# Optimization experiments

Measured on AMD Instinct MI355X. Metric: run time of the kernel, lower is better.

Reference implementation:

```python
import jax, jax.numpy as jnp
import numpy as np

NR, NS = 4, 3      # num_rotations, num_scales
RP, SP = 2, 2      # rotation_size, scale_size
K = 5              # kernel_size
PAD = 2
STRIDE = 1
NF = 9             # num basis functions (effective_size**2)


def setup_inputs() -> dict:
    key = jax.random.key(0)
    k1, k2, k3 = jax.random.split(key, 3)
    x = jax.random.normal(k1, (8, 16, NR * NS, 128, 128), dtype=jnp.float32)
    weight = jax.random.normal(k2, (16, 16, RP * SP, NF), dtype=jnp.float32) * 0.05
    basis = jax.random.normal(k3, (NF, NR * NS, K, K), dtype=jnp.float32)
    return {"x": x, "weight": weight, "basis": basis}


def reference(x, weight, basis):
    B, C, S, H, W = x.shape
    out_c, in_c, _, nf = weight.shape
    nrs = NR * NS
    # kernel synthesis: weight @ basis -> [nrs, out, in, RP*SP, K, K]
    kernel = jnp.einsum('oirf,fgxy->goirxy', weight, basis)
    kernel = kernel.reshape(nrs * out_c, in_c, RP, SP, K, K)
    # reshape input to [B, C, NR, NS, H, W]
    xg = x.reshape(B, C, NR, NS, H, W)
    # zero-pad scale axis at the end by SP-1
    xg = jnp.pad(xg, ((0, 0), (0, 0), (0, 0), (0, SP - 1), (0, 0), (0, 0)))
    # circular-pad rotation axis at the end by RP-1 (wrap from beginning)
    xg = jnp.concatenate([xg, xg[:, :, :RP - 1]], axis=2)
    out = None
    for i in range(RP):
        for j in range(SP):
            xs = xg[:, :, i:i + NR, j:j + NS]                     # [B,C,NR,NS,H,W]
            xs = xs.transpose(0, 2, 3, 1, 4, 5).reshape(B, nrs * C, H, W)
            o = jax.lax.conv_general_dilated(
                xs, kernel[:, :, i, j],
                window_strides=(STRIDE, STRIDE),
                padding=[(PAD, PAD), (PAD, PAD)],
                feature_group_count=nrs,
                dimension_numbers=('NCHW', 'OIHW', 'NCHW'))
            out = o if out is None else out + o
    B_, C_, H_, W_ = out.shape
    out = out.reshape(B_, nrs, out_c, H_, W_).transpose(0, 2, 1, 3, 4)
    return out
```

## Files before the change

kernel.cpp:

```cpp
#include <hip/hip_runtime.h>


#define NRS 12
#define CIN 16
#define COUT 16
#define HW 128
#define IMG (HW*HW)
#define ICSTRIDE (NRS*IMG)
#define HALO_H 36
#define HALO_W 20
#define NPIX (HALO_H*HALO_W)
#define HALFBYTES (NPIX*8*2)
#define ROWB (HALO_W*16)

typedef __bf16 bf16x8 __attribute__((ext_vector_type(8)));
typedef float  f32x4  __attribute__((ext_vector_type(4)));

__device__ __forceinline__ unsigned short f2bf(float f) {
    unsigned u = __builtin_bit_cast(unsigned, f);
    u += 0x7fffu + ((u >> 16) & 1u);
    return (unsigned short)(u >> 16);
}

__global__ void build_kc(const float* __restrict__ wgt, const float* __restrict__ basis,
                         unsigned short* __restrict__ kc) {
    int idx = blockIdx.x * 256 + threadIdx.x;
    const int total = 12 * 4 * 13 * 16 * 32;
    if (idx >= total) return;
    int k  = idx & 31;
    int possel = k >> 4, ic = k & 15;
    int o  = (idx >> 5) & 15;
    int t2 = idx >> 9;
    int pp = t2 % 13;
    int gr = t2 / 13;
    int rbase = gr & 3, g = gr >> 2;
    int pos = 2 * pp + possel;
    float s = 0.f;
    if (pos < 25) {
        int xk = pos / 5, yk = pos - 5 * xk;
        #pragma unroll
        for (int f = 0; f < 9; ++f)
            s = fmaf(wgt[((o * CIN + ic) * 4 + rbase) * 9 + f],
                     basis[((f * NRS + g) * 5 + xk) * 5 + yk], s);
    }
    kc[idx] = f2bf(s);
}

__global__ __launch_bounds__(256, 2)
void conv_mfma(const float* __restrict__ x, const unsigned short* __restrict__ kc,
               float* __restrict__ out) {
    const int b   = blockIdx.z;
    const int r0  = blockIdx.y;
    const int th0 = (blockIdx.x >> 3) * 32;
    const int tw0 = (blockIdx.x & 7) * 16;

    const int t    = threadIdx.x;
    const int lane = t & 63;
    const int wave = t >> 6;
    const int n    = lane & 15;
    const int q    = lane >> 4;
    const int possel = q >> 1;
    const int half_  = q & 1;

    __shared__ uint4 xs4[(2 * HALFBYTES) / 16];
    char* xsc = (char*)xs4;

    int boff[13];
    #pragma unroll
    for (int pp = 0; pp < 13; ++pp) {
        int pos = 2 * pp + possel; if (pos > 24) pos = 24;
        int dx = pos / 5, dy = pos - 5 * dx;
        boff[pp] = half_ * HALFBYTES + dx * ROWB + (n + dy) * 16;
    }
    const int aoff = n * 32 + q * 8;

    f32x4 acc[3][8];
    #pragma unroll
    for (int s0 = 0; s0 < 3; ++s0)
        #pragma unroll
        for (int pg = 0; pg < 8; ++pg) acc[s0][pg] = (f32x4){0.f, 0.f, 0.f, 0.f};

    #pragma unroll 1
    for (int i = 0; i < 2; ++i) {
        int rr = r0 + i; if (rr >= 4) rr -= 4;
        #pragma unroll
        for (int ss = 0; ss < 3; ++ss) {
            const int sin_ = rr * 3 + ss;
            const float* xb = x + ((size_t)b * CIN * NRS + sin_) * IMG;

            __syncthreads();
            for (int p = t; p < NPIX; p += 256) {
                int rl = p / HALO_W, cl = p - rl * HALO_W;
                int hh = th0 + rl - 2, ww = tw0 + cl - 2;
                bool ok = ((unsigned)hh < 128u) && ((unsigned)ww < 128u);
                const float* px = xb + hh * HW + ww;
                unsigned short v[16];
                #pragma unroll
                for (int ic = 0; ic < 16; ++ic) {
                    float f = 0.f;
                    if (ok) f = px[(size_t)ic * ICSTRIDE];
                    v[ic] = f2bf(f);
                }
                uint4 lo, hi;
                lo.x = v[0] | (v[1] << 16);  lo.y = v[2] | (v[3] << 16);
                lo.z = v[4] | (v[5] << 16);  lo.w = v[6] | (v[7] << 16);
                hi.x = v[8] | (v[9] << 16);  hi.y = v[10] | (v[11] << 16);
                hi.z = v[12] | (v[13] << 16); hi.w = v[14] | (v[15] << 16);
                *(uint4*)(xsc + p * 16)             = lo;
                *(uint4*)(xsc + HALFBYTES + p * 16) = hi;
            }
            __syncthreads();

            const unsigned short* kc0 = kc + (size_t)((r0 * 3 + ss) * 4 + 2 * i) * (13 * 512);
            const unsigned short* kc1 = kc + (size_t)((r0 * 3 + ss - 1) * 4 + 2 * i + 1) * (13 * 512);
            const char* wb = xsc + wave * 8 * ROWB;
            #pragma unroll
            for (int pp = 0; pp < 13; ++pp) {
                bf16x8 af0 = *(const bf16x8*)(kc0 + pp * 512 + aoff);
                bf16x8 af1;
                if (ss > 0) af1 = *(const bf16x8*)(kc1 + pp * 512 + aoff);
                const char* wp = wb + boff[pp];
                #pragma unroll
                for (int pg = 0; pg < 8; ++pg) {
                    bf16x8 bfv = *(const bf16x8*)(wp + pg * ROWB);
                    acc[ss][pg] = __builtin_amdgcn_mfma_f32_16x16x32_bf16(af0, bfv, acc[ss][pg], 0, 0, 0);
                    if (ss > 0)
                        acc[ss - 1][pg] = __builtin_amdgcn_mfma_f32_16x16x32_bf16(af1, bfv, acc[ss - 1][pg], 0, 0, 0);
                }
            }
        }
    }

    #pragma unroll
    for (int s0 = 0; s0 < 3; ++s0) {
        const size_t obase = ((size_t)b * COUT * NRS + (r0 * 3 + s0)) * IMG;
        #pragma unroll
        for (int pg = 0; pg < 8; ++pg) {
            int row = th0 + wave * 8 + pg;
            int col = tw0 + n;
            size_t pix = (size_t)row * HW + col;
            #pragma unroll
            for (int r = 0; r < 4; ++r) {
                int o = q * 4 + r;
                out[obase + (size_t)o * NRS * IMG + pix] = acc[s0][pg][r];
            }
        }
    }
}

extern "C" void kernel_launch(void* const* d_in, const int* in_sizes, int n_in,
                              void* d_out, int out_size, void* d_ws, size_t ws_size,
                              hipStream_t stream) {
    const float* x      = (const float*)d_in[0];
    const float* weight = (const float*)d_in[1];
    const float* basis  = (const float*)d_in[2];
    float* out = (float*)d_out;
    unsigned short* kc = (unsigned short*)d_ws;

    build_kc<<<dim3((12 * 4 * 13 * 16 * 32 + 255) / 256), dim3(256), 0, stream>>>(weight, basis, kc);
    conv_mfma<<<dim3(32, 4, 8), dim3(256), 0, stream>>>(x, kc, out);
}
```

Baseline: 296.1 us.

## Pre-convert input to padded bf16 layout and double-buffer LDS via async loads

Adds a pre-pass that converts x to bf16 in a zero-padded, channel-interleaved layout in workspace. The conv kernel then streams halo tiles straight into LDS with global_load_lds into double buffers, prefetching the next scale slice while MFMAs run on the current one. This is meant to remove the per-block fp32 gathers, conversions and boundary checks from the conv kernel and to overlap loads with compute. It costs an extra full pass over the input, a bf16 intermediate in global memory, and a fallback path when the workspace is too small.

```diff
diff --git a/kernel.cpp b/kernel.cpp
--- a/kernel.cpp
+++ b/kernel.cpp
@@ -7,11 +7,18 @@
 #define HW 128
 #define IMG (HW*HW)
 #define ICSTRIDE (NRS*IMG)
+
 #define HALO_H 36
 #define HALO_W 20
-#define NPIX (HALO_H*HALO_W)
-#define HALFBYTES (NPIX*8*2)
-#define ROWB (HALO_W*16)
+#define ROWB2 640
+#define NCHUNK 1440
+#define BUFB 24576
+#define PADW 132
+#define PADROWB (PADW*32)
+
+#define S_NPIX (HALO_H*HALO_W)
+#define S_HALFB (S_NPIX*16)
+#define S_ROWB (HALO_W*16)
 
 typedef __bf16 bf16x8 __attribute__((ext_vector_type(8)));
 typedef float  f32x4  __attribute__((ext_vector_type(4)));
@@ -46,8 +53,36 @@
     kc[idx] = f2bf(s);
 }
 
+__global__ void cvt_pad(const float* __restrict__ x, unsigned short* __restrict__ xbf) {
+    int idx = blockIdx.x * 256 + threadIdx.x;
+    const int total = 8 * 12 * PADW * PADW;
+    if (idx >= total) return;
+    int wp = idx % PADW;
+    int t1 = idx / PADW;
+    int hp = t1 % PADW;
+    int bs = t1 / PADW;
+    int s  = bs % 12, bb = bs / 12;
+    int h = hp - 2, w = wp - 2;
+    bool ok = ((unsigned)h < 128u) && ((unsigned)w < 128u);
+    const float* px = x + ((size_t)bb * 192 + s) * IMG + h * HW + w;
+    unsigned short v[16];
+    #pragma unroll
+    for (int ic = 0; ic < 16; ++ic) {
+        float f = 0.f;
+        if (ok) f = px[(size_t)ic * ICSTRIDE];
+        v[ic] = f2bf(f);
+    }
+    uint4 lo, hi;
+    lo.x = v[0] | (v[1] << 16);  lo.y = v[2] | (v[3] << 16);
+    lo.z = v[4] | (v[5] << 16);  lo.w = v[6] | (v[7] << 16);
+    hi.x = v[8] | (v[9] << 16);  hi.y = v[10] | (v[11] << 16);
+    hi.z = v[12] | (v[13] << 16); hi.w = v[14] | (v[15] << 16);
+    *(uint4*)(xbf + (size_t)idx * 16)     = lo;
+    *(uint4*)(xbf + (size_t)idx * 16 + 8) = hi;
+}
+
 __global__ __launch_bounds__(256, 2)
-void conv_mfma(const float* __restrict__ x, const unsigned short* __restrict__ kc,
+void conv_fast(const unsigned short* __restrict__ xbf, const unsigned short* __restrict__ kc,
                float* __restrict__ out) {
     const int b   = blockIdx.z;
     const int r0  = blockIdx.y;
@@ -62,15 +97,26 @@
     const int possel = q >> 1;
     const int half_  = q & 1;
 
-    __shared__ uint4 xs4[(2 * HALFBYTES) / 16];
+    __shared__ uint4 xs4[(2 * BUFB) / 16];
     char* xsc = (char*)xs4;
+
+    int soff[6];
+    #pragma unroll
+    for (int j = 0; j < 6; ++j) {
+        int c = wave * 384 + j * 64 + lane;
+        if (c < NCHUNK) {
+            int rl = c / 40, rem = c - rl * 40;
+            int hf = rem / 20, cl = rem - hf * 20;
+            soff[j] = rl * PADROWB + cl * 32 + hf * 16;
+        } else soff[j] = 0;
+    }
 
     int boff[13];
     #pragma unroll
     for (int pp = 0; pp < 13; ++pp) {
         int pos = 2 * pp + possel; if (pos > 24) pos = 24;
         int dx = pos / 5, dy = pos - 5 * dx;
-        boff[pp] = half_ * HALFBYTES + dx * ROWB + (n + dy) * 16;
+        boff[pp] = dx * ROWB2 + half_ * 320 + (n + dy) * 16;
     }
     const int aoff = n * 32 + q * 8;
 
@@ -79,17 +125,133 @@
     for (int s0 = 0; s0 < 3; ++s0)
         #pragma unroll
         for (int pg = 0; pg < 8; ++pg) acc[s0][pg] = (f32x4){0.f, 0.f, 0.f, 0.f};
+
+    const char* xb0 = (const char*)xbf;
+    const size_t tileoff = ((size_t)th0 * PADW + tw0) * 32;
+
+    {
+        const char* sb = xb0 + ((size_t)(b * 12 + r0 * 3) * PADW * PADW) * 32 + tileoff;
+        char* lb = xsc + wave * 6144;
+        #pragma unroll
+        for (int j = 0; j < 6; ++j)
+            __builtin_amdgcn_global_load_lds(
+                (const __attribute__((address_space(1))) void*)(sb + soff[j]),
+                (__attribute__((address_space(3))) void*)(lb + j * 1024), 16, 0, 0);
+    }
+    __syncthreads();
+    int cur = 0;
 
     #pragma unroll 1
     for (int i = 0; i < 2; ++i) {
         int rr = r0 + i; if (rr >= 4) rr -= 4;
+        int rrn = rr + 1; if (rrn >= 4) rrn -= 4;
+        #pragma unroll
+        for (int ss = 0; ss < 3; ++ss) {
+            if (i == 0 || ss < 2) {
+                int sin_next = (ss < 2) ? (rr * 3 + ss + 1) : (rrn * 3);
+                const char* sb = xb0 + ((size_t)(b * 12 + sin_next) * PADW * PADW) * 32 + tileoff;
+                char* lb = xsc + (cur ^ 1) * BUFB + wave * 6144;
+                #pragma unroll
+                for (int j = 0; j < 6; ++j)
+                    __builtin_amdgcn_global_load_lds(
+                        (const __attribute__((address_space(1))) void*)(sb + soff[j]),
+                        (__attribute__((address_space(3))) void*)(lb + j * 1024), 16, 0, 0);
+            }
+
+            const unsigned short* kc0 = kc + (size_t)((r0 * 3 + ss) * 4 + 2 * i) * (13 * 512);
+            const char* wb = xsc + cur * BUFB + wave * 8 * ROWB2;
+            if (ss > 0) {
+                const unsigned short* kc1 = kc + (size_t)((r0 * 3 + ss - 1) * 4 + 2 * i + 1) * (13 * 512);
+                #pragma unroll
+                for (int pp = 0; pp < 13; ++pp) {
+                    bf16x8 af0 = *(const bf16x8*)(kc0 + pp * 512 + aoff);
+                    bf16x8 af1 = *(const bf16x8*)(kc1 + pp * 512 + aoff);
+                    const char* wp = wb + boff[pp];
+                    #pragma unroll
+                    for (int pg = 0; pg < 8; ++pg) {
+                        bf16x8 bfv = *(const bf16x8*)(wp + pg * ROWB2);
+                        acc[ss][pg]     = __builtin_amdgcn_mfma_f32_16x16x32_bf16(af0, bfv, acc[ss][pg], 0, 0, 0);
+                        acc[ss - 1][pg] = __builtin_amdgcn_mfma_f32_16x16x32_bf16(af1, bfv, acc[ss - 1][pg], 0, 0, 0);
+                    }
+                }
+            } else {
+                #pragma unroll
+                for (int pp = 0; pp < 13; ++pp) {
+                    bf16x8 af0 = *(const bf16x8*)(kc0 + pp * 512 + aoff);
+                    const char* wp = wb + boff[pp];
+                    #pragma unroll
+                    for (int pg = 0; pg < 8; ++pg) {
+                        bf16x8 bfv = *(const bf16x8*)(wp + pg * ROWB2);
+                        acc[ss][pg] = __builtin_amdgcn_mfma_f32_16x16x32_bf16(af0, bfv, acc[ss][pg], 0, 0, 0);
+                    }
+                }
+            }
+            __syncthreads();
+            cur ^= 1;
+        }
+    }
+
+    #pragma unroll
+    for (int s0 = 0; s0 < 3; ++s0) {
+        const size_t obase = ((size_t)b * COUT * NRS + (r0 * 3 + s0)) * IMG;
+        #pragma unroll
+        for (int pg = 0; pg < 8; ++pg) {
+            int row = th0 + wave * 8 + pg;
+            int col = tw0 + n;
+            size_t pix = (size_t)row * HW + col;
+            #pragma unroll
+            for (int r = 0; r < 4; ++r) {
+                int o = q * 4 + r;
+                out[obase + (size_t)o * NRS * IMG + pix] = acc[s0][pg][r];
+            }
+        }
+    }
+}
+
+__global__ __launch_bounds__(256, 2)
+void conv_slow(const float* __restrict__ x, const unsigned short* __restrict__ kc,
+               float* __restrict__ out) {
+    const int b   = blockIdx.z;
+    const int r0  = blockIdx.y;
+    const int th0 = (blockIdx.x >> 3) * 32;
+    const int tw0 = (blockIdx.x & 7) * 16;
+
+    const int t    = threadIdx.x;
+    const int lane = t & 63;
+    const int wave = t >> 6;
+    const int n    = lane & 15;
+    const int q    = lane >> 4;
+    const int possel = q >> 1;
+    const int half_  = q & 1;
+
+    __shared__ uint4 xs4[(2 * S_HALFB) / 16];
+    char* xsc = (char*)xs4;
+
+    int boff[13];
+    #pragma unroll
+    for (int pp = 0; pp < 13; ++pp) {
+        int pos = 2 * pp + possel; if (pos > 24) pos = 24;
+        int dx = pos / 5, dy = pos - 5 * dx;
+        boff[pp] = half_ * S_HALFB + dx * S_ROWB + (n + dy) * 16;
+    }
+    const int aoff = n * 32 + q * 8;
+
+    f32x4 acc[3][8];
+    #pragma unroll
+    for (int s0 = 0; s0 < 3; ++s0)
+        #pragma unroll
+        for (int pg = 0; pg < 8; ++pg) acc[s0][pg] = (f32x4){0.f, 0.f, 0.f, 0.f};
+
+    #pragma unroll 1
+    for (int i = 0; i < 2; ++i) {
+        int rr = r0 + i; if (rr >= 4) rr -= 4;
         #pragma unroll
         for (int ss = 0; ss < 3; ++ss) {
             const int sin_ = rr * 3 + ss;
             const float* xb = x + ((size_t)b * CIN * NRS + sin_) * IMG;
 
             __syncthreads();
-            for (int p = t; p < NPIX; p += 256) {
+            for (int p = t; p < S_NPIX; p += 256) {
                 int rl = p / HALO_W, cl = p - rl * HALO_W;
                 int hh = th0 + rl - 2, ww = tw0 + cl - 2;
                 bool ok = ((unsigned)hh < 128u) && ((unsigned)ww < 128u);
@@ -106,14 +268,14 @@
                 lo.z = v[4] | (v[5] << 16);  lo.w = v[6] | (v[7] << 16);
                 hi.x = v[8] | (v[9] << 16);  hi.y = v[10] | (v[11] << 16);
                 hi.z = v[12] | (v[13] << 16); hi.w = v[14] | (v[15] << 16);
-                *(uint4*)(xsc + p * 16)             = lo;
-                *(uint4*)(xsc + HALFBYTES + p * 16) = hi;
+                *(uint4*)(xsc + p * 16)           = lo;
+                *(uint4*)(xsc + S_HALFB + p * 16) = hi;
             }
             __syncthreads();
 
             const unsigned short* kc0 = kc + (size_t)((r0 * 3 + ss) * 4 + 2 * i) * (13 * 512);
             const unsigned short* kc1 = kc + (size_t)((r0 * 3 + ss - 1) * 4 + 2 * i + 1) * (13 * 512);
-            const char* wb = xsc + wave * 8 * ROWB;
+            const char* wb = xsc + wave * 8 * S_ROWB;
             #pragma unroll
             for (int pp = 0; pp < 13; ++pp) {
                 bf16x8 af0 = *(const bf16x8*)(kc0 + pp * 512 + aoff);
@@ -122,7 +284,7 @@
                 const char* wp = wb + boff[pp];
                 #pragma unroll
                 for (int pg = 0; pg < 8; ++pg) {
-                    bf16x8 bfv = *(const bf16x8*)(wp + pg * ROWB);
+                    bf16x8 bfv = *(const bf16x8*)(wp + pg * S_ROWB);
                     acc[ss][pg] = __builtin_amdgcn_mfma_f32_16x16x32_bf16(af0, bfv, acc[ss][pg], 0, 0, 0);
                     if (ss > 0)
                         acc[ss - 1][pg] = __builtin_amdgcn_mfma_f32_16x16x32_bf16(af1, bfv, acc[ss - 1][pg], 0, 0, 0);
@@ -158,5 +320,14 @@
     unsigned short* kc = (unsigned short*)d_ws;
 
     build_kc<<<dim3((12 * 4 * 13 * 16 * 32 + 255) / 256), dim3(256), 0, stream>>>(weight, basis, kc);
-    conv_mfma<<<dim3(32, 4, 8), dim3(256), 0, stream>>>(x, kc, out);
-}
+
+    const size_t xbf_off = 655360;
+    const size_t xbf_bytes = (size_t)8 * 12 * PADW * PADW * 32;
+    if (ws_size >= xbf_off + xbf_bytes) {
+        unsigned short* xbf = (unsigned short*)((char*)d_ws + xbf_off);
+        cvt_pad<<<dim3((8 * 12 * PADW * PADW + 255) / 256), dim3(256), 0, stream>>>(x, xbf);
+        conv_fast<<<dim3(32, 4, 8), dim3(256), 0, stream>>>(xbf, kc, out);
+    } else {
+        conv_slow<<<dim3(32, 4, 8), dim3(256), 0, stream>>>(x, kc, out);
+    }
+}
```

After: 253.7 us. 1.17x faster.
